# Optimization experiments

Hardware: AMD Instinct MI355X
Metric: run time of the kernel (lower is better)

Reference implementation:

```python
import jax, jax.numpy as jnp
import numpy as np


def _hconv(x, src, eid, W, b, num_nodes, num_edges, att=None, hattr=None):
    """PyG HypergraphConv (heads=1, concat=True), optional node-mode attention.
    src: node index per incidence; eid: hyperedge index per incidence."""
    F = W.shape[0]
    xw = x @ W.T                                  # [N, F]
    alpha = None
    if att is not None:
        he = hattr @ W.T                          # [num_edges, F]
        # (cat([x_i, e_j]) * att).sum(-1) == x_i@att[:F] + e_j@att[F:]
        a = (xw @ att[:F])[src] + (he @ att[F:])[eid]   # [nnz]
        a = jnp.where(a > 0, a, 0.2 * a)          # leaky_relu(0.2)
        # node-mode softmax: normalize over incidences sharing the same hyperedge
        amax = jax.ops.segment_max(a, eid, num_segments=num_edges)
        ex = jnp.exp(a - amax[eid])
        denom = jax.ops.segment_sum(ex, eid, num_segments=num_edges)
        alpha = ex / denom[eid]
    ones = jnp.ones(src.shape[0], xw.dtype)
    Dn = jax.ops.segment_sum(ones, src, num_segments=num_nodes)   # node degree
    Dinv = jnp.where(Dn > 0, 1.0 / Dn, 0.0)
    Bn = jax.ops.segment_sum(ones, eid, num_segments=num_edges)   # edge degree
    Binv = jnp.where(Bn > 0, 1.0 / Bn, 0.0)
    # node -> hyperedge
    msg = Binv[eid][:, None] * xw[src]            # [nnz, F]
    if alpha is not None:
        msg = alpha[:, None] * msg
    efeat = jax.ops.segment_sum(msg, eid, num_segments=num_edges)
    # hyperedge -> node
    msg2 = Dinv[src][:, None] * efeat[eid]
    if alpha is not None:
        msg2 = alpha[:, None] * msg2
    return jax.ops.segment_sum(msg2, src, num_segments=num_nodes) + b


def setup_inputs() -> dict:
    key = jax.random.key(0)
    ks = jax.random.split(key, 13)
    D, M, Vc, Vm, F = 512, 1024, 2000, 2000, 64
    return {
        "c_it": jax.random.randint(ks[0], (D,), 0, Vc),
        "medicine_it": jax.random.randint(ks[1], (M,), 0, Vm),
        "c_embeddings": jax.random.normal(ks[2], (Vc, F), jnp.float32),
        "m_embeddings": jax.random.normal(ks[3], (Vm, F), jnp.float32),
        "pe0": jax.random.normal(ks[4], (Vc, F), jnp.float32),
        "pe1": jax.random.normal(ks[5], (Vm, F), jnp.float32),
        "conv_w": jax.random.normal(ks[6], (F, F), jnp.float32) / np.sqrt(F),
        "conv_b": jax.random.normal(ks[7], (F,), jnp.float32) * 0.02,
        "gat_w": jax.random.normal(ks[8], (F, F), jnp.float32) / np.sqrt(F),
        "gat_b": jax.random.normal(ks[9], (F,), jnp.float32) * 0.02,
        "gat_att": jax.random.normal(ks[10], (2 * F,), jnp.float32) / np.sqrt(2 * F),
        "hyperedge_attr": jax.random.normal(ks[11], (D, F), jnp.float32),
        "lin_w": jax.random.normal(ks[12], (F, 2 * F), jnp.float32) / np.sqrt(2 * F),
    }


def reference(c_it, medicine_it, c_embeddings, m_embeddings, pe0, pe1,
              conv_w, conv_b, gat_w, gat_b, gat_att, hyperedge_attr, lin_w):
    D = c_it.shape[0]
    M = medicine_it.shape[0]
    # single-hyperedge graphs over diseases and over meds
    dia_feat = _hconv(c_embeddings[c_it], jnp.arange(D), jnp.zeros(D, jnp.int32),
                      conv_w, conv_b, D, 1)
    med_feat = _hconv(m_embeddings[medicine_it], jnp.arange(M), jnp.zeros(M, jnp.int32),
                      conv_w, conv_b, M, 1)
    # dual hypergraph: hyperedge e = {disease e} U {all meds}
    comb = jnp.concatenate([c_embeddings[c_it], m_embeddings[medicine_it]], axis=0)  # [D+M, F]
    src = jnp.concatenate([jnp.arange(D)[:, None],
                           jnp.broadcast_to(jnp.arange(D, D + M), (D, M))],
                          axis=1).reshape(-1)                    # [D*(M+1)]
    eid = jnp.repeat(jnp.arange(D), M + 1)                       # [D*(M+1)]
    dm_feat = _hconv(comb, src, eid, gat_w, gat_b, D + M, D,
                     att=gat_att, hattr=hyperedge_attr)
    rep = jnp.concatenate([jnp.concatenate([dm_feat[:D], dia_feat], axis=1),
                           jnp.concatenate([dm_feat[D:], med_feat], axis=1)], axis=0)
    rep = rep @ lin_w.T                                          # [D+M, 64]
    # resi_output: vectorized sum over index loops
    i1 = (pe0[c_it].sum(0) + rep[:D].sum(0)).reshape(1, 1, -1)
    i2 = (pe1[medicine_it].sum(0) + rep[D:].sum(0)).reshape(1, 1, -1)
    return (i1, i2)
```

## Files before the change

### kernel.cpp

```cpp
#include <hip/hip_runtime.h>
#include <hip/hip_bf16.h>

#define D_N 512
#define M_N 1024
#define F_N 64
#define L2E 1.442695041f

__device__ __forceinline__ float wred_sum(float p) {
#pragma unroll
    for (int off = 32; off > 0; off >>= 1) p += __shfl_xor(p, off, 64);
    return p;
}

__device__ __forceinline__ float proj_col(const float* __restrict__ gw,
                                          const float* __restrict__ att,
                                          int lane) {
    float acc = 0.f;
#pragma unroll
    for (int k = 0; k < 64; ++k)
        acc += att[k] * gw[k * 64 + lane];
    return acc;
}

__global__ __launch_bounds__(512) void kprep(
    const int* __restrict__ c_it, const int* __restrict__ m_it,
    const float* __restrict__ c_emb, const float* __restrict__ m_emb,
    const float* __restrict__ pe0, const float* __restrict__ pe1,
    const float* __restrict__ gat_w, const float* __restrict__ gat_att,
    const float* __restrict__ hattr,
    float* __restrict__ umed, float* __restrict__ uc, float* __restrict__ v,
    float* __restrict__ pp)
{
    __shared__ __align__(16) float qs[64];
    __shared__ float redA[8][64], redB[8][64];
    const int b = blockIdx.x, tid = threadIdx.x;
    const int w = tid >> 6, lane = tid & 63;

    if (b < 48) {
        if (w == 0) qs[lane] = proj_col(gat_w, gat_att, lane);
        __syncthreads();
        const int* idx; const float* ta; const float* tb;
        float* dout; int base_r, oA, oB;
        if (b < 16) { idx = c_it; ta = pe0; tb = c_emb; dout = uc;
                      base_r = b * 32; oA = b; oB = 16 + b; }
        else { int g2 = b - 16; idx = m_it; ta = pe1; tb = m_emb; dout = umed;
               base_r = g2 * 32; oA = 32 + g2; oB = 64 + g2; }
        const int r0 = base_r + w * 4;
        float a = 0.f, bb = 0.f;
#pragma unroll
        for (int j = 0; j < 4; ++j) {
            const int row = r0 + j;
            const int r = idx[row];
            float av = ta[(size_t)r * F_N + lane];
            float bv = tb[(size_t)r * F_N + lane];
            a += av; bb += bv;
            float d = wred_sum(bv * qs[lane]);
            if (lane == 0) dout[row] = L2E * d;
        }
        redA[w][lane] = a; redB[w][lane] = bb;
        __syncthreads();
        if (w == 0) {
            float sa = 0.f, sbv = 0.f;
#pragma unroll
            for (int i = 0; i < 8; ++i) { sa += redA[i][lane]; sbv += redB[i][lane]; }
            pp[oA * 64 + lane] = sa;
            pp[oB * 64 + lane] = sbv;
        }
    } else {
        if (w == 0) qs[lane] = proj_col(gat_w, gat_att + 64, lane);
        __syncthreads();
        const int r0 = (b - 48) * 32 + w * 4;
#pragma unroll
        for (int j = 0; j < 4; ++j) {
            const int row = r0 + j;
            float hv = hattr[(size_t)row * F_N + lane];
            float d = wred_sum(hv * qs[lane]);
            if (lane == 0) v[row] = L2E * d;
        }
    }
}

__global__ __launch_bounds__(512) void kedge(
    const int* __restrict__ c_it, const float* __restrict__ c_emb,
    const float* __restrict__ umed_g, const float* __restrict__ uc,
    const float* __restrict__ v,
    float* __restrict__ c1f, float* __restrict__ c2f,
    float* __restrict__ e1dp, float* __restrict__ e2dp)
{
    __shared__ float umed[M_N];
    __shared__ float redA[8][64], redB[8][64];
    const int b = blockIdx.x, tid = threadIdx.x;
    const int w = tid >> 6, lane = tid & 63;

    umed[tid] = umed_g[tid];
    umed[tid + 512] = umed_g[tid + 512];
    __syncthreads();

    float accA = 0.f, accB = 0.f;
#pragma unroll
    for (int ee = 0; ee < 4; ++ee) {
        const int e = b * 32 + w * 4 + ee;
        const float ve = v[e];
        float s = 0.f;
#pragma unroll
        for (int i = 0; i < 16; ++i) {
            float a = umed[i * 64 + lane] + ve;
            a = fmaxf(a, 0.2f * a);
            s += exp2f(a);
        }
        s = wred_sum(s);
        float asf = uc[e] + ve; asf = fmaxf(asf, 0.2f * asf);
        const float exs = exp2f(asf);
        const float denom = s + exs;
        const float asel = exs / denom;
        const float rd = 1.f / (denom * (float)(M_N + 1));
        if (lane == 0) {
            c1f[e] = asel * rd;
            c2f[e] = (1.f - asel) * rd;
        }
        const float w1a = asel * rd * exs;
        const float w2a = (1.f - asel) * rd * exs;
        const float xe = c_emb[(size_t)c_it[e] * F_N + lane];
        accA += w1a * xe;
        accB += w2a * xe;
    }
    redA[w][lane] = accA; redB[w][lane] = accB;
    __syncthreads();
    if (w == 0) {
        float sa = 0.f, sbv = 0.f;
#pragma unroll
        for (int i = 0; i < 8; ++i) { sa += redA[i][lane]; sbv += redB[i][lane]; }
        e1dp[b * 64 + lane] = sa;
        e2dp[b * 64 + lane] = sbv;
    }
}

__global__ __launch_bounds__(512) void kmed(
    const int* __restrict__ m_it, const float* __restrict__ m_emb,
    const float* __restrict__ umed_g, const float* __restrict__ v,
    const float* __restrict__ c1f, const float* __restrict__ c2f,
    float* __restrict__ e1p, float* __restrict__ e2p)
{
    __shared__ float sV[D_N], sC1[D_N], sC2[D_N];
    __shared__ float sUm[32], sG1[32], sG2[32];
    __shared__ float redA[8][64], redB[8][64];
    const int b = blockIdx.x, tid = threadIdx.x;
    const int w = tid >> 6, lane = tid & 63;
    const int m_base = b * 32;

    sV[tid] = v[tid]; sC1[tid] = c1f[tid]; sC2[tid] = c2f[tid];
    if (tid < 32) sUm[tid] = umed_g[m_base + tid];
    __syncthreads();

    {
        const int mi = tid >> 4, l16 = tid & 15;
        const float um = sUm[mi];
        float gA = 0.f, gB = 0.f;
#pragma unroll 4
        for (int i = 0; i < 32; ++i) {
            int e = l16 + i * 16;
            float a = um + sV[e];
            a = fmaxf(a, 0.2f * a);
            float ex = exp2f(a);
            gA += sC1[e] * ex;
            gB += sC2[e] * ex;
        }
#pragma unroll
        for (int off = 1; off < 16; off <<= 1) {
            gA += __shfl_xor(gA, off, 64);
            gB += __shfl_xor(gB, off, 64);
        }
        if (l16 == 0) { sG1[mi] = gA; sG2[mi] = gB; }
    }
    __syncthreads();
    float a1 = 0.f, a2 = 0.f;
#pragma unroll
    for (int j = 0; j < 4; ++j) {
        int ml = w * 4 + j;
        float x = m_emb[(size_t)m_it[m_base + ml] * F_N + lane];
        a1 += sG1[ml] * x;
        a2 += sG2[ml] * x;
    }
    redA[w][lane] = a1; redB[w][lane] = a2;
    __syncthreads();
    if (w == 0) {
        float sa = 0.f, sbv = 0.f;
#pragma unroll
        for (int i = 0; i < 8; ++i) { sa += redA[i][lane]; sbv += redB[i][lane]; }
        e1p[b * 64 + lane] = sa;
        e2p[b * 64 + lane] = sbv;
    }
}

__global__ __launch_bounds__(256) void kfin(
    const float* __restrict__ conv_w, const float* __restrict__ conv_b,
    const float* __restrict__ gat_w, const float* __restrict__ gat_b,
    const float* __restrict__ lin_w,
    const float* __restrict__ pp,
    const float* __restrict__ e1p, const float* __restrict__ e2p,
    const float* __restrict__ e1dp, const float* __restrict__ e2dp,
    float* __restrict__ out)
{
    __shared__ float sE1[64], sE2[64], sP0[64], sP1[64], sMC[64], sMM[64];
    __shared__ float sS1[64], sS2[64];
    __shared__ float sRepD[128], sRepM[128];
    __shared__ float sWt[64 * 65];
    __shared__ float sLt[128 * 65];
    const int tid = threadIdx.x, w = tid >> 6, lane = tid & 63;

    if (w == 0) {
        float a = 0.f;
#pragma unroll
        for (int i = 0; i < 32; ++i) a += e1p[i * 64 + lane];
#pragma unroll
        for (int i = 0; i < 16; ++i) a += e1dp[i * 64 + lane];
        sE1[lane] = a;
    } else if (w == 1) {
        float a = 0.f;
#pragma unroll
        for (int i = 0; i < 32; ++i) a += e2p[i * 64 + lane];
#pragma unroll
        for (int i = 0; i < 16; ++i) a += e2dp[i * 64 + lane];
        sE2[lane] = a;
    } else if (w == 2) {
        float a = 0.f, c = 0.f;
#pragma unroll
        for (int i = 0; i < 16; ++i) { a += pp[i * 64 + lane]; c += pp[(16 + i) * 64 + lane]; }
        sP0[lane] = a; sMC[lane] = c * (1.f / (float)D_N);
    } else {
        float a = 0.f, c = 0.f;
#pragma unroll
        for (int i = 0; i < 32; ++i) { a += pp[(32 + i) * 64 + lane]; c += pp[(64 + i) * 64 + lane]; }
        sP1[lane] = a; sMM[lane] = c * (1.f / (float)M_N);
    }
    for (int i = tid; i < 4096; i += 256)
        sWt[(i & 63) * 65 + (i >> 6)] = gat_w[i];
    for (int i = tid; i < 8192; i += 256) {
        int k = i >> 7, j = i & 127;
        sLt[j * 65 + k] = lin_w[i];
    }
    __syncthreads();
    if (tid < 64) {
        float s1 = 0.f, s2 = 0.f;
#pragma unroll 8
        for (int j = 0; j < 64; ++j) {
            s1 += sE1[j] * sWt[j * 65 + lane];
            s2 += sE2[j] * sWt[j * 65 + lane];
        }
        sS1[lane] = s1;
        sS2[lane] = s2 * (1.f / (float)D_N);
    }
    __syncthreads();
    for (int i = tid; i < 4096; i += 256)
        sWt[(i & 63) * 65 + (i >> 6)] = conv_w[i];
    __syncthreads();
    if (tid < 64) {
        float dia = conv_b[lane], med = conv_b[lane];
#pragma unroll 8
        for (int j = 0; j < 64; ++j) {
            dia += sMC[j] * sWt[j * 65 + lane];
            med += sMM[j] * sWt[j * 65 + lane];
        }
        sRepD[lane]      = sS1[lane] + (float)D_N * gat_b[lane];
        sRepD[64 + lane] = (float)D_N * dia;
        sRepM[lane]      = sS2[lane] + (float)M_N * gat_b[lane];
        sRepM[64 + lane] = (float)M_N * med;
    }
    __syncthreads();
    if (tid < 64) {
        float o1 = sP0[lane], o2 = sP1[lane];
#pragma unroll 8
        for (int j = 0; j < 128; ++j) {
            o1 += sRepD[j] * sLt[j * 65 + lane];
            o2 += sRepM[j] * sLt[j * 65 + lane];
        }
        out[lane] = o1;
        out[64 + lane] = o2;
    }
}

extern "C" void kernel_launch(void* const* d_in, const int* in_sizes, int n_in,
                              void* d_out, int out_size, void* d_ws, size_t ws_size,
                              hipStream_t stream) {
    const int*   c_it    = (const int*)d_in[0];
    const int*   m_it    = (const int*)d_in[1];
    const float* c_emb   = (const float*)d_in[2];
    const float* m_emb   = (const float*)d_in[3];
    const float* pe0     = (const float*)d_in[4];
    const float* pe1     = (const float*)d_in[5];
    const float* conv_w  = (const float*)d_in[6];
    const float* conv_b  = (const float*)d_in[7];
    const float* gat_w   = (const float*)d_in[8];
    const float* gat_b   = (const float*)d_in[9];
    const float* gat_att = (const float*)d_in[10];
    const float* hattr   = (const float*)d_in[11];
    const float* lin_w   = (const float*)d_in[12];
    float* out = (float*)d_out;

    float* ws   = (float*)d_ws;
    float* umed = ws;
    float* uc   = umed + M_N;
    float* v    = uc + D_N;
    float* c1f  = v + D_N;
    float* c2f  = c1f + D_N;
    float* pp   = c2f + D_N;
    float* e1p  = pp + 96 * 64;
    float* e2p  = e1p + 32 * 64;
    float* e1dp = e2p + 32 * 64;
    float* e2dp = e1dp + 16 * 64;

    kprep<<<64, 512, 0, stream>>>(c_it, m_it, c_emb, m_emb, pe0, pe1,
                                  gat_w, gat_att, hattr, umed, uc, v, pp);
    kedge<<<16, 512, 0, stream>>>(c_it, c_emb, umed, uc, v,
                                  c1f, c2f, e1dp, e2dp);
    kmed<<<32, 512, 0, stream>>>(m_it, m_emb, umed, v, c1f, c2f, e1p, e2p);
    kfin<<<1, 256, 0, stream>>>(conv_w, conv_b, gat_w, gat_b, lin_w,
                                pp, e1p, e2p, e1dp, e2dp, out);
}
```

Measured before the change: 27.39 us.

## Fuse edge and medicine kernels by recomputing softmax denominators per block

```diff
diff --git a/kernel.cpp b/kernel.cpp
--- a/kernel.cpp
+++ b/kernel.cpp
@@ -80,115 +80,124 @@
     }
 }
 
-__global__ __launch_bounds__(512) void kedge(
-    const int* __restrict__ c_it, const float* __restrict__ c_emb,
-    const float* __restrict__ umed_g, const float* __restrict__ uc,
-    const float* __restrict__ v,
-    float* __restrict__ c1f, float* __restrict__ c2f,
+__global__ __launch_bounds__(512) void kcomb(
+    const int* __restrict__ c_it, const int* __restrict__ m_it,
+    const float* __restrict__ c_emb, const float* __restrict__ m_emb,
+    const float* __restrict__ umed_g, const float* __restrict__ uc_g,
+    const float* __restrict__ v_g,
+    float* __restrict__ e1p, float* __restrict__ e2p,
     float* __restrict__ e1dp, float* __restrict__ e2dp)
 {
-    __shared__ float umed[M_N];
+    __shared__ __align__(16) float umed[M_N];
+    __shared__ float sUc[D_N], sV[D_N];
+    __shared__ float sC1[D_N], sC2[D_N];
+    __shared__ float sG1[32], sG2[32];
     __shared__ float redA[8][64], redB[8][64];
     const int b = blockIdx.x, tid = threadIdx.x;
     const int w = tid >> 6, lane = tid & 63;
 
     umed[tid] = umed_g[tid];
     umed[tid + 512] = umed_g[tid + 512];
-    __syncthreads();
-
-    float accA = 0.f, accB = 0.f;
-#pragma unroll
-    for (int ee = 0; ee < 4; ++ee) {
-        const int e = b * 32 + w * 4 + ee;
-        const float ve = v[e];
-        float s = 0.f;
-#pragma unroll
-        for (int i = 0; i < 16; ++i) {
-            float a = umed[i * 64 + lane] + ve;
-            a = fmaxf(a, 0.2f * a);
-            s += exp2f(a);
-        }
-        s = wred_sum(s);
-        float asf = uc[e] + ve; asf = fmaxf(asf, 0.2f * asf);
-        const float exs = exp2f(asf);
-        const float denom = s + exs;
-        const float asel = exs / denom;
-        const float rd = 1.f / (denom * (float)(M_N + 1));
-        if (lane == 0) {
-            c1f[e] = asel * rd;
-            c2f[e] = (1.f - asel) * rd;
-        }
-        const float w1a = asel * rd * exs;
-        const float w2a = (1.f - asel) * rd * exs;
-        const float xe = c_emb[(size_t)c_it[e] * F_N + lane];
-        accA += w1a * xe;
-        accB += w2a * xe;
-    }
-    redA[w][lane] = accA; redB[w][lane] = accB;
-    __syncthreads();
-    if (w == 0) {
-        float sa = 0.f, sbv = 0.f;
-#pragma unroll
-        for (int i = 0; i < 8; ++i) { sa += redA[i][lane]; sbv += redB[i][lane]; }
-        e1dp[b * 64 + lane] = sa;
-        e2dp[b * 64 + lane] = sbv;
-    }
-}
-
-__global__ __launch_bounds__(512) void kmed(
-    const int* __restrict__ m_it, const float* __restrict__ m_emb,
-    const float* __restrict__ umed_g, const float* __restrict__ v,
-    const float* __restrict__ c1f, const float* __restrict__ c2f,
-    float* __restrict__ e1p, float* __restrict__ e2p)
-{
-    __shared__ float sV[D_N], sC1[D_N], sC2[D_N];
-    __shared__ float sUm[32], sG1[32], sG2[32];
-    __shared__ float redA[8][64], redB[8][64];
-    const int b = blockIdx.x, tid = threadIdx.x;
-    const int w = tid >> 6, lane = tid & 63;
-    const int m_base = b * 32;
-
-    sV[tid] = v[tid]; sC1[tid] = c1f[tid]; sC2[tid] = c2f[tid];
-    if (tid < 32) sUm[tid] = umed_g[m_base + tid];
-    __syncthreads();
-
-    {
-        const int mi = tid >> 4, l16 = tid & 15;
-        const float um = sUm[mi];
-        float gA = 0.f, gB = 0.f;
+    sUc[tid] = uc_g[tid];
+    sV[tid] = v_g[tid];
+    __syncthreads();
+
+    if (b < 32) {
+        {
+            const float ve = sV[tid];
+            const float4* u4 = (const float4*)umed;
+            float s = 0.f;
+#pragma unroll 8
+            for (int i = 0; i < 256; ++i) {
+                float4 uv = u4[i];
+                float a0 = uv.x + ve; a0 = fmaxf(a0, 0.2f * a0); s += exp2f(a0);
+                float a1 = uv.y + ve; a1 = fmaxf(a1, 0.2f * a1); s += exp2f(a1);
+                float a2 = uv.z + ve; a2 = fmaxf(a2, 0.2f * a2); s += exp2f(a2);
+                float a3 = uv.w + ve; a3 = fmaxf(a3, 0.2f * a3); s += exp2f(a3);
+            }
+            float asf = sUc[tid] + ve; asf = fmaxf(asf, 0.2f * asf);
+            const float exs = exp2f(asf);
+            const float denom = s + exs;
+            const float asel = exs / denom;
+            const float rd = 1.f / (denom * (float)(M_N + 1));
+            sC1[tid] = asel * rd;
+            sC2[tid] = (1.f - asel) * rd;
+        }
+        __syncthreads();
+        const int m_base = b * 32;
+        {
+            const int mi = tid >> 4, l16 = tid & 15;
+            const float um = umed[m_base + mi];
+            float gA = 0.f, gB = 0.f;
 #pragma unroll 4
-        for (int i = 0; i < 32; ++i) {
-            int e = l16 + i * 16;
-            float a = um + sV[e];
-            a = fmaxf(a, 0.2f * a);
-            float ex = exp2f(a);
-            gA += sC1[e] * ex;
-            gB += sC2[e] * ex;
-        }
-#pragma unroll
-        for (int off = 1; off < 16; off <<= 1) {
-            gA += __shfl_xor(gA, off, 64);
-            gB += __shfl_xor(gB, off, 64);
-        }
-        if (l16 == 0) { sG1[mi] = gA; sG2[mi] = gB; }
-    }
-    __syncthreads();
-    float a1 = 0.f, a2 = 0.f;
-#pragma unroll
-    for (int j = 0; j < 4; ++j) {
-        int ml = w * 4 + j;
-        float x = m_emb[(size_t)m_it[m_base + ml] * F_N + lane];
-        a1 += sG1[ml] * x;
-        a2 += sG2[ml] * x;
-    }
-    redA[w][lane] = a1; redB[w][lane] = a2;
-    __syncthreads();
-    if (w == 0) {
-        float sa = 0.f, sbv = 0.f;
-#pragma unroll
-        for (int i = 0; i < 8; ++i) { sa += redA[i][lane]; sbv += redB[i][lane]; }
-        e1p[b * 64 + lane] = sa;
-        e2p[b * 64 + lane] = sbv;
+            for (int i = 0; i < 32; ++i) {
+                int e = l16 + i * 16;
+                float a = um + sV[e];
+                a = fmaxf(a, 0.2f * a);
+                float ex = exp2f(a);
+                gA += sC1[e] * ex;
+                gB += sC2[e] * ex;
+            }
+#pragma unroll
+            for (int off = 1; off < 16; off <<= 1) {
+                gA += __shfl_xor(gA, off, 64);
+                gB += __shfl_xor(gB, off, 64);
+            }
+            if (l16 == 0) { sG1[mi] = gA; sG2[mi] = gB; }
+        }
+        __syncthreads();
+        float a1 = 0.f, a2 = 0.f;
+#pragma unroll
+        for (int j = 0; j < 4; ++j) {
+            int ml = w * 4 + j;
+            float x = m_emb[(size_t)m_it[m_base + ml] * F_N + lane];
+            a1 += sG1[ml] * x;
+            a2 += sG2[ml] * x;
+        }
+        redA[w][lane] = a1; redB[w][lane] = a2;
+        __syncthreads();
+        if (w == 0) {
+            float sa = 0.f, sbv = 0.f;
+#pragma unroll
+            for (int i = 0; i < 8; ++i) { sa += redA[i][lane]; sbv += redB[i][lane]; }
+            e1p[b * 64 + lane] = sa;
+            e2p[b * 64 + lane] = sbv;
+        }
+    } else {
+        const int sbb = b - 32;
+        float accA = 0.f, accB = 0.f;
+#pragma unroll 2
+        for (int ee = 0; ee < 16; ++ee) {
+            const int e = sbb * 128 + w * 16 + ee;
+            const float ve = sV[e];
+            float s = 0.f;
+#pragma unroll
+            for (int i = 0; i < 16; ++i) {
+                float a = umed[i * 64 + lane] + ve;
+                a = fmaxf(a, 0.2f * a);
+                s += exp2f(a);
+            }
+            s = wred_sum(s);
+            float asf = sUc[e] + ve; asf = fmaxf(asf, 0.2f * asf);
+            const float exs = exp2f(asf);
+            const float denom = s + exs;
+            const float asel = exs / denom;
+            const float rd = 1.f / (denom * (float)(M_N + 1));
+            const float w1a = asel * rd * exs;
+            const float w2a = (1.f - asel) * rd * exs;
+            const float xe = c_emb[(size_t)c_it[e] * F_N + lane];
+            accA += w1a * xe;
+            accB += w2a * xe;
+        }
+        redA[w][lane] = accA; redB[w][lane] = accB;
+        __syncthreads();
+        if (w == 0) {
+            float sa = 0.f, sbv = 0.f;
+#pragma unroll
+            for (int i = 0; i < 8; ++i) { sa += redA[i][lane]; sbv += redB[i][lane]; }
+            e1dp[sbb * 64 + lane] = sa;
+            e2dp[sbb * 64 + lane] = sbv;
+        }
     }
 }
 
@@ -213,14 +222,14 @@
 #pragma unroll
         for (int i = 0; i < 32; ++i) a += e1p[i * 64 + lane];
 #pragma unroll
-        for (int i = 0; i < 16; ++i) a += e1dp[i * 64 + lane];
+        for (int i = 0; i < 4; ++i) a += e1dp[i * 64 + lane];
         sE1[lane] = a;
     } else if (w == 1) {
         float a = 0.f;
 #pragma unroll
         for (int i = 0; i < 32; ++i) a += e2p[i * 64 + lane];
 #pragma unroll
-        for (int i = 0; i < 16; ++i) a += e2dp[i * 64 + lane];
+        for (int i = 0; i < 4; ++i) a += e2dp[i * 64 + lane];
         sE2[lane] = a;
     } else if (w == 2) {
         float a = 0.f, c = 0.f;
@@ -301,19 +310,16 @@
     float* umed = ws;
     float* uc   = umed + M_N;
     float* v    = uc + D_N;
-    float* c1f  = v + D_N;
-    float* c2f  = c1f + D_N;
-    float* pp   = c2f + D_N;
+    float* pp   = v + D_N;
     float* e1p  = pp + 96 * 64;
     float* e2p  = e1p + 32 * 64;
     float* e1dp = e2p + 32 * 64;
-    float* e2dp = e1dp + 16 * 64;
+    float* e2dp = e1dp + 4 * 64;
 
     kprep<<<64, 512, 0, stream>>>(c_it, m_it, c_emb, m_emb, pe0, pe1,
                                   gat_w, gat_att, hattr, umed, uc, v, pp);
-    kedge<<<16, 512, 0, stream>>>(c_it, c_emb, umed, uc, v,
-                                  c1f, c2f, e1dp, e2dp);
-    kmed<<<32, 512, 0, stream>>>(m_it, m_emb, umed, v, c1f, c2f, e1p, e2p);
+    kcomb<<<36, 512, 0, stream>>>(c_it, m_it, c_emb, m_emb,
+                                  umed, uc, v, e1p, e2p, e1dp, e2dp);
     kfin<<<1, 256, 0, stream>>>(conv_w, conv_b, gat_w, gat_b, lin_w,
                                 pp, e1p, e2p, e1dp, e2dp, out);
 }
```

New measurement: 61.01 us. 123% more time.
